# Kernel optimization log

Measured on AMD Instinct MI355X. Metric: run time of the kernel, lower is better.

The kernel has to match this reference:

```python
import jax, jax.numpy as jnp
import numpy as np

L = 3; D = 128; H = 8; RBF = 16; SBF = 112
N = 60000; E = 300000; A = 8000; G = 256
EPS = 1e-8


def setup_inputs() -> dict:
    key = jax.random.key(0)
    ks = jax.random.split(key, 32)
    p = lambda i, shape: jax.random.normal(ks[i], shape, jnp.float32) * 0.05
    inp = {}
    inp['x'] = jax.random.normal(ks[0], (N, D), jnp.float32)
    inp['node_rbf'] = jax.random.uniform(ks[1], (N, RBF), jnp.float32)
    inp['edge_sbf'] = jax.random.uniform(ks[2], (E, SBF), jnp.float32)
    inp['edge_index'] = jax.random.randint(ks[3], (2, E), 0, N)
    inp['pair_atom_idx'] = jax.random.randint(ks[4], (E,), 0, A)
    inp['edge_index_0'] = jax.random.randint(ks[5], (N,), 0, A)
    inp['atom_batch'] = jnp.sort(jax.random.randint(ks[6], (A,), 0, G))
    inp['batch'] = jnp.sort(jax.random.randint(ks[7], (N,), 0, G))
    inp['edgenn_w1'] = p(8, (L, D, D)); inp['edgenn_b1'] = jnp.zeros((L, D))
    inp['edgenn_w2'] = p(9, (L, D, D)); inp['edgenn_b2'] = jnp.zeros((L, D))
    inp['conv_wq'] = p(10, (L, D, D)); inp['conv_wk'] = p(11, (L, D, D))
    inp['conv_wv'] = p(12, (L, D, D)); inp['conv_we'] = p(13, (L, D, D))
    inp['conv_wsbf'] = p(14, (L, SBF, D)); inp['conv_bsbf'] = jnp.zeros((L, D))
    inp['conv_wrbf'] = p(15, (L, RBF, D))
    inp['dense_w'] = p(16, (L, D, D)); inp['dense_b'] = jnp.zeros((L, D))
    inp['bf_w'] = p(17, (L, 2, D, D)); inp['bf_b'] = jnp.zeros((L, 2, D))
    inp['af_w'] = p(18, (L, 4, D, D)); inp['af_b'] = jnp.zeros((L, 4, D))
    inp['read_wrbf'] = p(19, (L + 1, RBF, D))
    inp['read_w1'] = p(20, (L + 1, D, D)); inp['read_b1'] = jnp.zeros((L + 1, D))
    inp['read_w2'] = p(21, (L + 1, D, D)); inp['read_b2'] = jnp.zeros((L + 1, D))
    inp['read_w3'] = p(22, (L + 1, D, 1)); inp['read_b3'] = jnp.zeros((L + 1, 1))
    return inp


def _forward(x, node_rbf, edge_sbf, edge_index, pair_atom_idx, edge_index_0,
             atom_batch, batch, edgenn_w1, edgenn_b1, edgenn_w2, edgenn_b2,
             conv_wq, conv_wk, conv_wv, conv_we, conv_wsbf, conv_bsbf, conv_wrbf,
             dense_w, dense_b, bf_w, bf_b, af_w, af_b,
             read_wrbf, read_w1, read_b1, read_w2, read_b2, read_w3, read_b3):
    segsum = jax.ops.segment_sum
    silu = jax.nn.silu
    src, dst = edge_index[0], edge_index[1]
    C = D // H

    def readout(i, h):
        # AtomWise: rbf-gated node features, scatter to atoms, small MLP -> [A,1]
        g = h * (node_rbf @ read_wrbf[i])
        atoms = segsum(g, edge_index_0, num_segments=A)
        a = silu(atoms @ read_w1[i] + read_b1[i])
        a = silu(a @ read_w2[i] + read_b2[i])
        return a @ read_w3[i] + read_b3[i]

    def res_block(h, w, b):
        # DimeNet-style ResidualLayer: x + act(lin2(act(lin1(x))))
        return h + silu(silu(h @ w[0] + b[0]) @ w[1] + b[1])

    def graph_norm(h):
        # batch-aware LayerNorm (graph mode, affine=False)
        cnt = segsum(jnp.ones((N,), h.dtype), batch, num_segments=G) * D
        mean = segsum(h.sum(-1), batch, num_segments=G) / cnt
        hc = h - mean[batch][:, None]
        var = segsum((hc * hc).sum(-1), batch, num_segments=G) / cnt
        return hc * jax.lax.rsqrt(var + EPS)[batch][:, None]

    out = x
    results = readout(0, out)
    for i in range(L):
        res0 = out
        atoms_rep = segsum(out, edge_index_0, num_segments=A)  # scatter_add to atoms
        ea = atoms_rep[pair_atom_idx]                           # gather per conv-edge
        ea = silu(ea @ edgenn_w1[i] + edgenn_b1[i]) @ edgenn_w2[i] + edgenn_b2[i]
        # SBFTransformerConv: TransformerConv with sbf-modulated messages + rbf gate
        q = (out @ conv_wq[i]).reshape(N, H, C)
        k = (out @ conv_wk[i]).reshape(N, H, C)
        v = (out @ conv_wv[i]).reshape(N, H, C)
        ek = (ea @ conv_we[i]).reshape(E, H, C)
        kj = k[src] + ek
        logit = (q[dst] * kj).sum(-1) / jnp.sqrt(jnp.asarray(C, out.dtype))  # [E,H]
        m = jax.ops.segment_max(logit, dst, num_segments=N)
        ex = jnp.exp(logit - m[dst])
        alpha = ex / (segsum(ex, dst, num_segments=N)[dst] + 1e-16)
        sw = (edge_sbf @ conv_wsbf[i] + conv_bsbf[i]).reshape(E, H, C)
        msg = (v[src] + ek) * alpha[:, :, None] * sw
        h = segsum(msg, dst, num_segments=N).reshape(N, D)
        out = h * (node_rbf @ conv_wrbf[i])
        out = graph_norm(out)
        out = res_block(out, bf_w[i], bf_b[i])
        out = silu(out @ dense_w[i] + dense_b[i])
        out = out + res0
        out = res_block(out, af_w[i, :2], af_b[i, :2])
        out = res_block(out, af_w[i, 2:], af_b[i, 2:])
        results = results + readout(i + 1, out)
    graphs = segsum(results, atom_batch, num_segments=G)  # [G,1]
    return graphs.reshape(-1) / L


def reference(x, node_rbf, edge_sbf, edge_index, pair_atom_idx, edge_index_0,
              atom_batch, batch, edgenn_w1, edgenn_b1, edgenn_w2, edgenn_b2,
              conv_wq, conv_wk, conv_wv, conv_we, conv_wsbf, conv_bsbf, conv_wrbf,
              dense_w, dense_b, bf_w, bf_b, af_w, af_b,
              read_wrbf, read_w1, read_b1, read_w2, read_b2, read_w3, read_b3):
    return _forward(x, node_rbf, edge_sbf, edge_index, pair_atom_idx, edge_index_0,
                    atom_batch, batch, edgenn_w1, edgenn_b1, edgenn_w2, edgenn_b2,
                    conv_wq, conv_wk, conv_wv, conv_we, conv_wsbf, conv_bsbf, conv_wrbf,
                    dense_w, dense_b, bf_w, bf_b, af_w, af_b,
                    read_wrbf, read_w1, read_b1, read_w2, read_b2, read_w3, read_b3)
```

## Files before the change

kernel.cpp:

```cpp
#include <hip/hip_runtime.h>
#include <math.h>

#define D    128
#define NH   8
#define CPH  16
#define RBFD 16
#define SBFD 112
#define LAYERS 3

typedef __attribute__((ext_vector_type(8))) short bf16x8;
typedef __attribute__((ext_vector_type(4))) float f32x4;

__device__ __forceinline__ float siluf(float x){ return x / (1.0f + __expf(-x)); }

__device__ __forceinline__ short f2bf(float f){
  union { float f; unsigned u; } v; v.f = f;
  unsigned r = v.u + 0x7FFFu + ((v.u >> 16) & 1u);
  return (short)(r >> 16);
}

template<int DIN, int ACT, bool GATHER, bool HASB, bool HASRES, bool PERM>
__global__ __launch_bounds__(256, 2) void k_gemm(
    const float* __restrict__ X, const int* __restrict__ gidx,
    const float* __restrict__ W, const float* __restrict__ bias,
    const float* res, float* __restrict__ Y, const int* __restrict__ operm, int M)
{
  __shared__ short Wt[128 * 128];
  if (DIN < 128){
    for (int i = threadIdx.x; i < 128 * 128; i += 256) Wt[i] = 0;
    __syncthreads();
  }
  for (int i = threadIdx.x; i < DIN * 128; i += 256){
    int k = i >> 7, c = i & 127;
    Wt[c * 128 + k] = f2bf(W[i]);
  }
  __syncthreads();

  const int lane = threadIdx.x & 63;
  const int wave = threadIdx.x >> 6;
  const int col0 = lane & 15;
  const int kg   = lane >> 4;

  bf16x8 Bf[8][4];
  #pragma unroll
  for (int ct = 0; ct < 8; ct++)
    #pragma unroll
    for (int s = 0; s < 4; s++)
      Bf[ct][s] = *(const bf16x8*)&Wt[(ct * 16 + col0) * 128 + s * 32 + kg * 8];

  float bs[8];
  if (HASB){
    #pragma unroll
    for (int ct = 0; ct < 8; ct++) bs[ct] = bias[ct * 16 + col0];
  }

  const long tiles = ((long)M + 63) >> 6;
  for (long t = blockIdx.x; t < tiles; t += gridDim.x){
    const long rbase = t * 64 + wave * 16;
    const long arow  = rbase + col0;
    long srow = 0;
    if (arow < M) srow = GATHER ? (long)gidx[arow] : arow;
    const float* Xp = X + srow * DIN;

    bf16x8 Af[4];
    #pragma unroll
    for (int s = 0; s < 4; s++){
      const int kb = s * 32 + kg * 8;
      bf16x8 a;
      if (DIN == 128 || kb + 8 <= DIN){
        float4 lo = *(const float4*)(Xp + kb);
        float4 hi = *(const float4*)(Xp + kb + 4);
        a[0]=f2bf(lo.x); a[1]=f2bf(lo.y); a[2]=f2bf(lo.z); a[3]=f2bf(lo.w);
        a[4]=f2bf(hi.x); a[5]=f2bf(hi.y); a[6]=f2bf(hi.z); a[7]=f2bf(hi.w);
      } else {
        #pragma unroll
        for (int j = 0; j < 8; j++) a[j] = 0;
      }
      Af[s] = a;
    }

    f32x4 acc[8];
    #pragma unroll
    for (int ct = 0; ct < 8; ct++){ acc[ct][0]=0.f; acc[ct][1]=0.f; acc[ct][2]=0.f; acc[ct][3]=0.f; }
    #pragma unroll
    for (int ct = 0; ct < 8; ct++)
      #pragma unroll
      for (int s = 0; s < 4; s++)
        acc[ct] = __builtin_amdgcn_mfma_f32_16x16x32_bf16(Af[s], Bf[ct][s], acc[ct], 0, 0, 0);

    #pragma unroll
    for (int r = 0; r < 4; r++){
      const long orow = rbase + kg * 4 + r;
      if (orow >= M) continue;
      const long wrow = PERM ? (long)operm[orow] : orow;
      #pragma unroll
      for (int ct = 0; ct < 8; ct++){
        const int c = ct * 16 + col0;
        float v = acc[ct][r];
        if (HASB) v += bs[ct];
        if (ACT)  v = siluf(v);
        if (HASRES) v += res[orow * D + c];
        Y[wrow * D + c] = v;
      }
    }
  }
}

__global__ __launch_bounds__(256, 2) void k_gemm2(
    const float* __restrict__ X, const int* __restrict__ gidx,
    const float* __restrict__ W1, const float* __restrict__ b1,
    const float* __restrict__ W2, const float* __restrict__ b2,
    float* __restrict__ Y, const int* __restrict__ operm, int M)
{
  __shared__ short W1t[128 * 128];
  __shared__ short W2t[128 * 128];
  __shared__ short Ts[64 * 128];
  for (int i = threadIdx.x; i < 128 * 128; i += 256){
    int k = i >> 7, c = i & 127;
    W1t[c * 128 + k] = f2bf(W1[i]);
    W2t[c * 128 + k] = f2bf(W2[i]);
  }
  __syncthreads();

  const int lane = threadIdx.x & 63;
  const int wave = threadIdx.x >> 6;
  const int col0 = lane & 15;
  const int kg   = lane >> 4;

  bf16x8 B1f[8][4];
  #pragma unroll
  for (int ct = 0; ct < 8; ct++)
    #pragma unroll
    for (int s = 0; s < 4; s++)
      B1f[ct][s] = *(const bf16x8*)&W1t[(ct * 16 + col0) * 128 + s * 32 + kg * 8];

  float bs1[8], bs2[8];
  #pragma unroll
  for (int ct = 0; ct < 8; ct++){ bs1[ct] = b1[ct * 16 + col0]; bs2[ct] = b2[ct * 16 + col0]; }

  const long tiles = ((long)M + 63) >> 6;
  for (long t = blockIdx.x; t < tiles; t += gridDim.x){
    const long rbase = t * 64 + wave * 16;
    const long arow  = rbase + col0;
    long srow = 0;
    if (arow < M) srow = (long)gidx[arow];
    const float* Xp = X + srow * D;

    bf16x8 Af[4];
    #pragma unroll
    for (int s = 0; s < 4; s++){
      const int kb = s * 32 + kg * 8;
      float4 lo = *(const float4*)(Xp + kb);
      float4 hi = *(const float4*)(Xp + kb + 4);
      bf16x8 a;
      a[0]=f2bf(lo.x); a[1]=f2bf(lo.y); a[2]=f2bf(lo.z); a[3]=f2bf(lo.w);
      a[4]=f2bf(hi.x); a[5]=f2bf(hi.y); a[6]=f2bf(hi.z); a[7]=f2bf(hi.w);
      Af[s] = a;
    }

    f32x4 acc[8];
    #pragma unroll
    for (int ct = 0; ct < 8; ct++){ acc[ct][0]=0.f; acc[ct][1]=0.f; acc[ct][2]=0.f; acc[ct][3]=0.f; }
    #pragma unroll
    for (int ct = 0; ct < 8; ct++)
      #pragma unroll
      for (int s = 0; s < 4; s++)
        acc[ct] = __builtin_amdgcn_mfma_f32_16x16x32_bf16(Af[s], B1f[ct][s], acc[ct], 0, 0, 0);

    #pragma unroll
    for (int ct = 0; ct < 8; ct++){
      const int c = ct * 16 + col0;
      #pragma unroll
      for (int r = 0; r < 4; r++){
        const int row = wave * 16 + kg * 4 + r;
        const int gg = (c >> 3) ^ (row & 7);
        Ts[row * 128 + gg * 8 + (c & 7)] = f2bf(siluf(acc[ct][r] + bs1[ct]));
      }
    }
    __syncthreads();

    const int row2 = wave * 16 + col0;
    bf16x8 A2f[4];
    #pragma unroll
    for (int s = 0; s < 4; s++){
      const int chunk = (s * 4 + kg) ^ (row2 & 7);
      A2f[s] = *(const bf16x8*)&Ts[row2 * 128 + chunk * 8];
    }
    __syncthreads();

    #pragma unroll
    for (int ct = 0; ct < 8; ct++){ acc[ct][0]=0.f; acc[ct][1]=0.f; acc[ct][2]=0.f; acc[ct][3]=0.f; }
    #pragma unroll
    for (int ct = 0; ct < 8; ct++){
      bf16x8 B2v[4];
      #pragma unroll
      for (int s = 0; s < 4; s++)
        B2v[s] = *(const bf16x8*)&W2t[(ct * 16 + col0) * 128 + s * 32 + kg * 8];
      #pragma unroll
      for (int s = 0; s < 4; s++)
        acc[ct] = __builtin_amdgcn_mfma_f32_16x16x32_bf16(A2f[s], B2v[s], acc[ct], 0, 0, 0);
    }

    #pragma unroll
    for (int r = 0; r < 4; r++){
      const long orow = rbase + kg * 4 + r;
      if (orow >= M) continue;
      const long wrow = (long)operm[orow];
      #pragma unroll
      for (int ct = 0; ct < 8; ct++){
        const int c = ct * 16 + col0;
        Y[wrow * D + c] = acc[ct][r] + bs2[ct];
      }
    }
  }
}

template<bool NORM>
__global__ __launch_bounds__(256, 2) void k_res2(
    const float* __restrict__ X,
    const float* __restrict__ W1, const float* __restrict__ b1,
    const float* __restrict__ W2, const float* __restrict__ b2,
    const int* __restrict__ batch, const float* __restrict__ meanG,
    const float* __restrict__ rstdG, float* __restrict__ Y, int M)
{
  __shared__ short W1t[128 * 128];
  __shared__ short W2t[128 * 128];
  __shared__ short Ts[64 * 128];
  for (int i = threadIdx.x; i < 128 * 128; i += 256){
    int k = i >> 7, c = i & 127;
    W1t[c * 128 + k] = f2bf(W1[i]);
    W2t[c * 128 + k] = f2bf(W2[i]);
  }
  __syncthreads();

  const int lane = threadIdx.x & 63;
  const int wave = threadIdx.x >> 6;
  const int col0 = lane & 15;
  const int kg   = lane >> 4;

  bf16x8 B1f[8][4];
  #pragma unroll
  for (int ct = 0; ct < 8; ct++)
    #pragma unroll
    for (int s = 0; s < 4; s++)
      B1f[ct][s] = *(const bf16x8*)&W1t[(ct * 16 + col0) * 128 + s * 32 + kg * 8];

  float bs1[8], bs2[8];
  #pragma unroll
  for (int ct = 0; ct < 8; ct++){ bs1[ct] = b1[ct * 16 + col0]; bs2[ct] = b2[ct * 16 + col0]; }

  const long tiles = ((long)M + 63) >> 6;
  for (long t = blockIdx.x; t < tiles; t += gridDim.x){
    const long rbase = t * 64 + wave * 16;
    const long arow  = rbase + col0;
    const float* Xp = X + (arow < M ? arow : 0) * D;
    float xm = 0.f, xr = 1.f;
    if (NORM && arow < M){ int g = batch[arow]; xm = meanG[g]; xr = rstdG[g]; }

    bf16x8 Af[4];
    #pragma unroll
    for (int s = 0; s < 4; s++){
      const int kb = s * 32 + kg * 8;
      float4 lo = *(const float4*)(Xp + kb);
      float4 hi = *(const float4*)(Xp + kb + 4);
      bf16x8 a;
      a[0]=f2bf((lo.x-xm)*xr); a[1]=f2bf((lo.y-xm)*xr); a[2]=f2bf((lo.z-xm)*xr); a[3]=f2bf((lo.w-xm)*xr);
      a[4]=f2bf((hi.x-xm)*xr); a[5]=f2bf((hi.y-xm)*xr); a[6]=f2bf((hi.z-xm)*xr); a[7]=f2bf((hi.w-xm)*xr);
      Af[s] = a;
    }

    f32x4 acc[8];
    #pragma unroll
    for (int ct = 0; ct < 8; ct++){ acc[ct][0]=0.f; acc[ct][1]=0.f; acc[ct][2]=0.f; acc[ct][3]=0.f; }
    #pragma unroll
    for (int ct = 0; ct < 8; ct++)
      #pragma unroll
      for (int s = 0; s < 4; s++)
        acc[ct] = __builtin_amdgcn_mfma_f32_16x16x32_bf16(Af[s], B1f[ct][s], acc[ct], 0, 0, 0);

    #pragma unroll
    for (int ct = 0; ct < 8; ct++){
      const int c = ct * 16 + col0;
      #pragma unroll
      for (int r = 0; r < 4; r++){
        const int row = wave * 16 + kg * 4 + r;
        const int gg = (c >> 3) ^ (row & 7);
        Ts[row * 128 + gg * 8 + (c & 7)] = f2bf(siluf(acc[ct][r] + bs1[ct]));
      }
    }
    __syncthreads();

    const int row2 = wave * 16 + col0;
    bf16x8 A2f[4];
    #pragma unroll
    for (int s = 0; s < 4; s++){
      const int chunk = (s * 4 + kg) ^ (row2 & 7);
      A2f[s] = *(const bf16x8*)&Ts[row2 * 128 + chunk * 8];
    }
    __syncthreads();

    #pragma unroll
    for (int ct = 0; ct < 8; ct++){ acc[ct][0]=0.f; acc[ct][1]=0.f; acc[ct][2]=0.f; acc[ct][3]=0.f; }
    #pragma unroll
    for (int ct = 0; ct < 8; ct++){
      bf16x8 B2v[4];
      #pragma unroll
      for (int s = 0; s < 4; s++)
        B2v[s] = *(const bf16x8*)&W2t[(ct * 16 + col0) * 128 + s * 32 + kg * 8];
      #pragma unroll
      for (int s = 0; s < 4; s++)
        acc[ct] = __builtin_amdgcn_mfma_f32_16x16x32_bf16(A2f[s], B2v[s], acc[ct], 0, 0, 0);
    }

    #pragma unroll
    for (int r = 0; r < 4; r++){
      const long orow = rbase + kg * 4 + r;
      if (orow >= M) continue;
      float rm = 0.f, rr = 1.f;
      if (NORM){ int g = batch[orow]; rm = meanG[g]; rr = rstdG[g]; }
      #pragma unroll
      for (int ct = 0; ct < 8; ct++){
        const int c = ct * 16 + col0;
        float base = X[orow * D + c];
        if (NORM) base = (base - rm) * rr;
        Y[orow * D + c] = base + siluf(acc[ct][r] + bs2[ct]);
      }
    }
  }
}

__global__ __launch_bounds__(256, 2) void k_read2(
    const float* __restrict__ X,
    const float* __restrict__ W1, const float* __restrict__ b1,
    const float* __restrict__ W2, const float* __restrict__ b2,
    const float* __restrict__ w3, const float* __restrict__ b3,
    float* __restrict__ results, int M)
{
  __shared__ short W1t[128 * 128];
  __shared__ short W2t[128 * 128];
  __shared__ short Ts[64 * 128];
  for (int i = threadIdx.x; i < 128 * 128; i += 256){
    int k = i >> 7, c = i & 127;
    W1t[c * 128 + k] = f2bf(W1[i]);
    W2t[c * 128 + k] = f2bf(W2[i]);
  }
  __syncthreads();

  const int lane = threadIdx.x & 63;
  const int wave = threadIdx.x >> 6;
  const int col0 = lane & 15;
  const int kg   = lane >> 4;

  bf16x8 B1f[8][4];
  #pragma unroll
  for (int ct = 0; ct < 8; ct++)
    #pragma unroll
    for (int s = 0; s < 4; s++)
      B1f[ct][s] = *(const bf16x8*)&W1t[(ct * 16 + col0) * 128 + s * 32 + kg * 8];

  float bs1[8], bs2[8], w3v[8];
  #pragma unroll
  for (int ct = 0; ct < 8; ct++){
    bs1[ct] = b1[ct * 16 + col0];
    bs2[ct] = b2[ct * 16 + col0];
    w3v[ct] = w3[ct * 16 + col0];
  }
  const float b3v = b3[0];

  const long tiles = ((long)M + 63) >> 6;
  for (long t = blockIdx.x; t < tiles; t += gridDim.x){
    const long rbase = t * 64 + wave * 16;
    const long arow  = rbase + col0;
    const float* Xp = X + (arow < M ? arow : 0) * D;

    bf16x8 Af[4];
    #pragma unroll
    for (int s = 0; s < 4; s++){
      const int kb = s * 32 + kg * 8;
      float4 lo = *(const float4*)(Xp + kb);
      float4 hi = *(const float4*)(Xp + kb + 4);
      bf16x8 a;
      a[0]=f2bf(lo.x); a[1]=f2bf(lo.y); a[2]=f2bf(lo.z); a[3]=f2bf(lo.w);
      a[4]=f2bf(hi.x); a[5]=f2bf(hi.y); a[6]=f2bf(hi.z); a[7]=f2bf(hi.w);
      Af[s] = a;
    }

    f32x4 acc[8];
    #pragma unroll
    for (int ct = 0; ct < 8; ct++){ acc[ct][0]=0.f; acc[ct][1]=0.f; acc[ct][2]=0.f; acc[ct][3]=0.f; }
    #pragma unroll
    for (int ct = 0; ct < 8; ct++)
      #pragma unroll
      for (int s = 0; s < 4; s++)
        acc[ct] = __builtin_amdgcn_mfma_f32_16x16x32_bf16(Af[s], B1f[ct][s], acc[ct], 0, 0, 0);

    #pragma unroll
    for (int ct = 0; ct < 8; ct++){
      const int c = ct * 16 + col0;
      #pragma unroll
      for (int r = 0; r < 4; r++){
        const int row = wave * 16 + kg * 4 + r;
        const int gg = (c >> 3) ^ (row & 7);
        Ts[row * 128 + gg * 8 + (c & 7)] = f2bf(siluf(acc[ct][r] + bs1[ct]));
      }
    }
    __syncthreads();

    const int row2 = wave * 16 + col0;
    bf16x8 A2f[4];
    #pragma unroll
    for (int s = 0; s < 4; s++){
      const int chunk = (s * 4 + kg) ^ (row2 & 7);
      A2f[s] = *(const bf16x8*)&Ts[row2 * 128 + chunk * 8];
    }
    __syncthreads();

    #pragma unroll
    for (int ct = 0; ct < 8; ct++){ acc[ct][0]=0.f; acc[ct][1]=0.f; acc[ct][2]=0.f; acc[ct][3]=0.f; }
    #pragma unroll
    for (int ct = 0; ct < 8; ct++){
      bf16x8 B2v[4];
      #pragma unroll
      for (int s = 0; s < 4; s++)
        B2v[s] = *(const bf16x8*)&W2t[(ct * 16 + col0) * 128 + s * 32 + kg * 8];
      #pragma unroll
      for (int s = 0; s < 4; s++)
        acc[ct] = __builtin_amdgcn_mfma_f32_16x16x32_bf16(A2f[s], B2v[s], acc[ct], 0, 0, 0);
    }

    #pragma unroll
    for (int r = 0; r < 4; r++){
      float vr = 0.f;
      #pragma unroll
      for (int ct = 0; ct < 8; ct++)
        vr += siluf(acc[ct][r] + bs2[ct]) * w3v[ct];
      #pragma unroll
      for (int off = 1; off < 16; off <<= 1) vr += __shfl_xor(vr, off, 64);
      const long orow = rbase + kg * 4 + r;
      if (col0 == 0 && orow < M) results[orow] += vr + b3v;
    }
  }
}

__global__ void k_hist(const int* __restrict__ idx, int* __restrict__ cnt, int M)
{
  for (long i = (long)blockIdx.x * 256 + threadIdx.x; i < M; i += (long)gridDim.x * 256)
    atomicAdd(&cnt[idx[i]], 1);
}

__global__ void k_scan(const int* __restrict__ cnt, int* __restrict__ rowptr, int M)
{
  __shared__ int buf[1024];
  const int tid = threadIdx.x;
  const int PT = 16;
  int carry = 0;
  for (int base = 0; base < M; base += 1024 * PT){
    int loc[PT]; int s = 0;
    #pragma unroll
    for (int j = 0; j < PT; j++){
      int i = base + tid * PT + j;
      loc[j] = (i < M) ? cnt[i] : 0;
      s += loc[j];
    }
    buf[tid] = s; __syncthreads();
    for (int off = 1; off < 1024; off <<= 1){
      int t = (tid >= off) ? buf[tid - off] : 0;
      __syncthreads();
      buf[tid] += t;
      __syncthreads();
    }
    int run = buf[tid] - s + carry;
    carry += buf[1023];
    __syncthreads();
    #pragma unroll
    for (int j = 0; j < PT; j++){
      int i = base + tid * PT + j;
      if (i < M) rowptr[i] = run;
      run += loc[j];
    }
  }
  if (tid == 0) rowptr[M] = carry;
}

__global__ void k_fill(const int* __restrict__ idx, const int* __restrict__ rowptr,
                       int* __restrict__ cursor, int* __restrict__ ids, int M)
{
  for (long i = (long)blockIdx.x * 256 + threadIdx.x; i < M; i += (long)gridDim.x * 256){
    int sgm = idx[i];
    int pos = atomicAdd(&cursor[sgm], 1);
    ids[rowptr[sgm] + pos] = (int)i;
  }
}

__global__ void k_invsrc(const int* __restrict__ eids, const int* __restrict__ srcA,
                         int* __restrict__ invD, int* __restrict__ srcCSR, int E_)
{
  for (long i = (long)blockIdx.x * 256 + threadIdx.x; i < E_; i += (long)gridDim.x * 256){
    int e = eids[i];
    invD[e] = (int)i;
    srcCSR[i] = srcA[e];
  }
}

__global__ __launch_bounds__(256) void k_gather_sum(
    const float* __restrict__ X, const int* __restrict__ rowptr,
    const int* __restrict__ ids, float* __restrict__ Yat, int A_)
{
  const int lane = threadIdx.x & 63;
  const int wv   = threadIdx.x >> 6;
  for (long a = (long)blockIdx.x * 4 + wv; a < A_; a += (long)gridDim.x * 4){
    int beg = rowptr[a], end = rowptr[a + 1];
    float a0 = 0.f, a1 = 0.f;
    for (int i = beg; i < end; i++){
      const float* xp = X + (long)ids[i] * D;
      a0 += xp[lane]; a1 += xp[lane + 64];
    }
    Yat[a * D + lane] = a0; Yat[a * D + lane + 64] = a1;
  }
}

__global__ __launch_bounds__(256) void k_gather_gate_sum(
    const float* __restrict__ X, const float* __restrict__ rbf,
    const float* __restrict__ Wr, const int* __restrict__ rowptr,
    const int* __restrict__ ids, float* __restrict__ Yat, int A_)
{
  __shared__ float Wrs[RBFD * D];
  for (int i = threadIdx.x; i < RBFD * D; i += 256) Wrs[i] = Wr[i];
  __syncthreads();
  const int lane = threadIdx.x & 63;
  const int wv   = threadIdx.x >> 6;
  for (long a = (long)blockIdx.x * 4 + wv; a < A_; a += (long)gridDim.x * 4){
    int beg = rowptr[a], end = rowptr[a + 1];
    float a0 = 0.f, a1 = 0.f;
    for (int i = beg; i < end; i++){
      long n = ids[i];
      const float* xp = X + n * D;
      const float* rb = rbf + n * RBFD;
      float g0 = 0.f, g1 = 0.f;
      #pragma unroll
      for (int r = 0; r < RBFD; r++){
        float rv = rb[r];
        g0 += rv * Wrs[r * D + lane];
        g1 += rv * Wrs[r * D + lane + 64];
      }
      a0 += xp[lane] * g0; a1 += xp[lane + 64] * g1;
    }
    Yat[a * D + lane] = a0; Yat[a * D + lane + 64] = a1;
  }
}

__device__ __forceinline__ void attn_step(long i, const int* __restrict__ srcCSR,
    const float* __restrict__ k, const float* __restrict__ v,
    const float* __restrict__ ek, const float* __restrict__ sw, int lane,
    float q0, float q1, float& m0, float& m1, float& l0, float& l1, float& a0, float& a1)
{
  const long s = srcCSR[i];
  const float* kp = k + s * D;
  const float* vp = v + s * D;
  const float* ep = ek + i * D;
  const float* sp = sw + i * D;
  float e0 = ep[lane], e1 = ep[lane + 64];
  float t0 = q0 * (kp[lane] + e0), t1 = q1 * (kp[lane + 64] + e1);
  #pragma unroll
  for (int off = 1; off < 16; off <<= 1){
    t0 += __shfl_xor(t0, off, 64);
    t1 += __shfl_xor(t1, off, 64);
  }
  t0 *= 0.25f; t1 *= 0.25f;
  float u0 = (vp[lane] + e0) * sp[lane];
  float u1 = (vp[lane + 64] + e1) * sp[lane + 64];
  float nm0 = fmaxf(m0, t0), nm1 = fmaxf(m1, t1);
  float sc0 = __expf(m0 - nm0), sc1 = __expf(m1 - nm1);
  float w0 = __expf(t0 - nm0), w1 = __expf(t1 - nm1);
  l0 = l0 * sc0 + w0;  a0 = a0 * sc0 + w0 * u0;  m0 = nm0;
  l1 = l1 * sc1 + w1;  a1 = a1 * sc1 + w1 * u1;  m1 = nm1;
}

__global__ __launch_bounds__(256) void k_attn(
    float* __restrict__ q, const float* __restrict__ k, const float* __restrict__ v,
    const float* __restrict__ ek, const float* __restrict__ sw,
    const int* __restrict__ rowptr, const int* __restrict__ srcCSR,
    const float* __restrict__ rbf, const float* __restrict__ Wr,
    const int* __restrict__ batch,
    double* __restrict__ sums, double* __restrict__ sumsq, int Nn)
{
  __shared__ float Wrs[RBFD * D];
  for (int i = threadIdx.x; i < RBFD * D; i += 256) Wrs[i] = Wr[i];
  __syncthreads();
  const int lane = threadIdx.x & 63;
  const int wv   = threadIdx.x >> 6;
  for (long d = (long)blockIdx.x * 4 + wv; d < Nn; d += (long)gridDim.x * 4){
    const int beg = rowptr[d], end = rowptr[d + 1];
    const float q0 = q[d * D + lane], q1 = q[d * D + lane + 64];
    float mA0=-1e30f, mA1=-1e30f, lA0=0.f, lA1=0.f, aA0=0.f, aA1=0.f;
    float mB0=-1e30f, mB1=-1e30f, lB0=0.f, lB1=0.f, aB0=0.f, aB1=0.f;
    int i = beg;
    for (; i + 1 < end; i += 2){
      attn_step(i,     srcCSR, k, v, ek, sw, lane, q0, q1, mA0, mA1, lA0, lA1, aA0, aA1);
      attn_step(i + 1, srcCSR, k, v, ek, sw, lane, q0, q1, mB0, mB1, lB0, lB1, aB0, aB1);
    }
    if (i < end)
      attn_step(i, srcCSR, k, v, ek, sw, lane, q0, q1, mA0, mA1, lA0, lA1, aA0, aA1);
    float nm0 = fmaxf(mA0, mB0), nm1 = fmaxf(mA1, mB1);
    float sA0 = __expf(mA0 - nm0), sB0 = __expf(mB0 - nm0);
    float sA1 = __expf(mA1 - nm1), sB1 = __expf(mB1 - nm1);
    float l0 = lA0 * sA0 + lB0 * sB0, l1 = lA1 * sA1 + lB1 * sB1;
    float a0 = aA0 * sA0 + aB0 * sB0, a1 = aA1 * sA1 + aB1 * sB1;
    a0 /= (l0 + 1e-16f); a1 /= (l1 + 1e-16f);
    const float* rb = rbf + d * RBFD;
    float g0 = 0.f, g1 = 0.f;
    #pragma unroll
    for (int r = 0; r < RBFD; r++){
      float rv = rb[r];
      g0 += rv * Wrs[r * D + lane];
      g1 += rv * Wrs[r * D + lane + 64];
    }
    a0 *= g0; a1 *= g1;
    q[d * D + lane] = a0; q[d * D + lane + 64] = a1;
    float ss = a0 + a1, qq = a0 * a0 + a1 * a1;
    #pragma unroll
    for (int off = 1; off < 64; off <<= 1){
      ss += __shfl_xor(ss, off, 64);
      qq += __shfl_xor(qq, off, 64);
    }
    if (lane == 0){
      int g = batch[d];
      atomicAdd(&sums[g], (double)ss);
      atomicAdd(&sumsq[g], (double)qq);
    }
  }
}

__global__ void k_count(const int* __restrict__ batch, int* __restrict__ cnt, int M)
{
  for (long i = (long)blockIdx.x * 256 + threadIdx.x; i < M; i += (long)gridDim.x * 256)
    atomicAdd(&cnt[batch[i]], 1);
}

__global__ void k_norm_final(const double* __restrict__ sums, const double* __restrict__ sumsq,
                             const int* __restrict__ cnt, float* __restrict__ meanG,
                             float* __restrict__ rstdG)
{
  int g = threadIdx.x;
  double c = (double)cnt[g] * (double)D;
  double mean = sums[g] / c;
  double var = sumsq[g] / c - mean * mean;
  meanG[g] = (float)mean;
  rstdG[g] = (float)(1.0 / sqrt(var + 1e-8));
}

__global__ void k_final(const float* __restrict__ results, const int* __restrict__ ab,
                        float* __restrict__ out, int A_)
{
  int i = blockIdx.x * 256 + threadIdx.x;
  if (i < A_) atomicAdd(&out[ab[i]], results[i] / 3.0f);
}

__global__ void k_w2e(const float* __restrict__ w2, const float* __restrict__ we,
                      float* __restrict__ W2e)
{
  int i = blockIdx.x >> 7;
  int r = blockIdx.x & 127;
  int c = threadIdx.x;
  const float* w2p = w2 + (size_t)i * D * D + (size_t)r * D;
  const float* wep = we + (size_t)i * D * D;
  float acc = 0.f;
  for (int j = 0; j < D; j++) acc += w2p[j] * wep[j * D + c];
  W2e[(size_t)i * D * D + (size_t)r * D + c] = acc;
}

__global__ void k_b2e(const float* __restrict__ b2, const float* __restrict__ we,
                      float* __restrict__ B2e)
{
  int i = blockIdx.x; int c = threadIdx.x;
  float acc = 0.f;
  for (int j = 0; j < D; j++) acc += b2[(size_t)i * D + j] * we[(size_t)i * D * D + j * D + c];
  B2e[(size_t)i * D + c] = acc;
}

extern "C" void kernel_launch(void* const* d_in, const int* in_sizes, int n_in,
                              void* d_out, int out_size, void* d_ws, size_t ws_size,
                              hipStream_t stream)
{
  const float* x          = (const float*)d_in[0];
  const float* node_rbf   = (const float*)d_in[1];
  const float* edge_sbf   = (const float*)d_in[2];
  const int*   edge_index = (const int*)d_in[3];
  const int*   pair_idx   = (const int*)d_in[4];
  const int*   eidx0      = (const int*)d_in[5];
  const int*   atom_batch = (const int*)d_in[6];
  const int*   batch      = (const int*)d_in[7];
  const float* edgenn_w1  = (const float*)d_in[8];
  const float* edgenn_b1  = (const float*)d_in[9];
  const float* edgenn_w2  = (const float*)d_in[10];
  const float* edgenn_b2  = (const float*)d_in[11];
  const float* conv_wq    = (const float*)d_in[12];
  const float* conv_wk    = (const float*)d_in[13];
  const float* conv_wv    = (const float*)d_in[14];
  const float* conv_we    = (const float*)d_in[15];
  const float* conv_wsbf  = (const float*)d_in[16];
  const float* conv_bsbf  = (const float*)d_in[17];
  const float* conv_wrbf  = (const float*)d_in[18];
  const float* dense_w    = (const float*)d_in[19];
  const float* dense_b    = (const float*)d_in[20];
  const float* bf_w       = (const float*)d_in[21];
  const float* bf_b       = (const float*)d_in[22];
  const float* af_w       = (const float*)d_in[23];
  const float* af_b       = (const float*)d_in[24];
  const float* read_wrbf  = (const float*)d_in[25];
  const float* read_w1    = (const float*)d_in[26];
  const float* read_b1    = (const float*)d_in[27];
  const float* read_w2    = (const float*)d_in[28];
  const float* read_b2    = (const float*)d_in[29];
  const float* read_w3    = (const float*)d_in[30];
  const float* read_b3    = (const float*)d_in[31];

  const int N = in_sizes[0] / D;
  const int E = in_sizes[4];
  const int A = in_sizes[6];
  const int G = out_size;

  char* p = (char*)d_ws;
  auto carve = [&](size_t bytes)->char*{ char* r = p; p += (bytes + 255) & ~(size_t)255; return r; };
  float*    EbufA   = (float*)carve((size_t)E * D * 4);
  float*    EbufB   = (float*)carve((size_t)E * D * 4);
  float*    ping0   = (float*)carve((size_t)N * D * 4);
  float*    ping1   = (float*)carve((size_t)N * D * 4);
  float*    bq      = (float*)carve((size_t)N * D * 4);
  float*    bk      = (float*)carve((size_t)N * D * 4);
  float*    bv      = (float*)carve((size_t)N * D * 4);
  float*    bufAtoms= (float*)carve((size_t)A * D * 4);
  float*    results = (float*)carve((size_t)A * 4);
  double*   sumG    = (double*)carve((size_t)G * 8);
  double*   sumsqG  = (double*)carve((size_t)G * 8);
  int*      cntG    = (int*)carve((size_t)G * 4);
  float*    meanG   = (float*)carve((size_t)G * 4);
  float*    rstdG   = (float*)carve((size_t)G * 4);
  float*    W2e     = (float*)carve((size_t)LAYERS * D * D * 4);
  float*    B2e     = (float*)carve((size_t)LAYERS * D * 4);
  int*      rowptrD = (int*)carve((size_t)(N + 1) * 4);
  int*      eidsD   = (int*)carve((size_t)E * 4);
  int*      invD    = (int*)carve((size_t)E * 4);
  int*      srcCSR  = (int*)carve((size_t)E * 4);
  int*      cntD    = (int*)carve((size_t)N * 4);
  int*      rowptrA = (int*)carve((size_t)(A + 1) * 4);
  int*      idsA    = (int*)carve((size_t)N * 4);
  int*      cntA    = (int*)carve((size_t)A * 4);

  const int* srcA = edge_index;
  const int* dstA = edge_index + E;

  auto ew_grid = [](long total){ long b = (total + 255) / 256; return (int)(b < 4096 ? b : 4096); };
  auto gemm_grid = [](int M){ long t = ((long)M + 63) / 64; return (int)(t < 1024 ? t : 1024); };
  const int gridAttn = (N + 3) / 4;
  const int gridAtom = (A + 3) / 4;

  hipMemsetAsync(cntG, 0, (size_t)G * 4, stream);
  hipMemsetAsync(results, 0, (size_t)A * 4, stream);
  hipMemsetAsync(d_out, 0, (size_t)G * 4, stream);
  k_count<<<ew_grid(N), 256, 0, stream>>>(batch, cntG, N);
  k_w2e<<<LAYERS * D, D, 0, stream>>>(edgenn_w2, conv_we, W2e);
  k_b2e<<<LAYERS, D, 0, stream>>>(edgenn_b2, conv_we, B2e);
  hipMemsetAsync(cntD, 0, (size_t)N * 4, stream);
  k_hist<<<ew_grid(E), 256, 0, stream>>>(dstA, cntD, E);
  k_scan<<<1, 1024, 0, stream>>>(cntD, rowptrD, N);
  hipMemsetAsync(cntD, 0, (size_t)N * 4, stream);
  k_fill<<<ew_grid(E), 256, 0, stream>>>(dstA, rowptrD, cntD, eidsD, E);
  k_invsrc<<<ew_grid(E), 256, 0, stream>>>(eidsD, srcA, invD, srcCSR, E);
  hipMemsetAsync(cntA, 0, (size_t)A * 4, stream);
  k_hist<<<ew_grid(N), 256, 0, stream>>>(eidx0, cntA, N);
  k_scan<<<1, 1024, 0, stream>>>(cntA, rowptrA, A);
  hipMemsetAsync(cntA, 0, (size_t)A * 4, stream);
  k_fill<<<ew_grid(N), 256, 0, stream>>>(eidx0, rowptrA, cntA, idsA, N);

  auto readout = [&](int i, const float* hbuf){
    k_gather_gate_sum<<<gridAtom, 256, 0, stream>>>(hbuf, node_rbf, read_wrbf + (size_t)i * RBFD * D,
                                                    rowptrA, idsA, bufAtoms, A);
    k_read2<<<gemm_grid(A), 256, 0, stream>>>(bufAtoms,
        read_w1 + (size_t)i*D*D, read_b1 + (size_t)i*D,
        read_w2 + (size_t)i*D*D, read_b2 + (size_t)i*D,
        read_w3 + (size_t)i*D, read_b3 + i, results, A);
  };

  readout(0, x);

  const float* cur = x;
  float* pp[2] = {ping0, ping1};
  for (int i = 0; i < LAYERS; i++){
    float* nxt = pp[i & 1];
    const size_t oDD = (size_t)i * D * D;
    k_gather_sum<<<gridAtom, 256, 0, stream>>>(cur, rowptrA, idsA, bufAtoms, A);
    k_gemm2<<<gemm_grid(E),256,0,stream>>>(bufAtoms, pair_idx, edgenn_w1 + oDD, edgenn_b1 + (size_t)i*D,
                                           W2e + oDD, B2e + (size_t)i*D, EbufB, invD, E);
    k_gemm<D,0,false,false,false,false><<<gemm_grid(N),256,0,stream>>>(cur, nullptr, conv_wq + oDD, nullptr, nullptr, bq, nullptr, N);
    k_gemm<D,0,false,false,false,false><<<gemm_grid(N),256,0,stream>>>(cur, nullptr, conv_wk + oDD, nullptr, nullptr, bk, nullptr, N);
    k_gemm<D,0,false,false,false,false><<<gemm_grid(N),256,0,stream>>>(cur, nullptr, conv_wv + oDD, nullptr, nullptr, bv, nullptr, N);
    k_gemm<SBFD,0,false,true,false,true><<<gemm_grid(E),256,0,stream>>>(edge_sbf, nullptr, conv_wsbf + (size_t)i*SBFD*D, conv_bsbf + (size_t)i*D, nullptr, EbufA, invD, E);
    hipMemsetAsync(sumG, 0, (size_t)G * 16, stream);
    k_attn<<<gridAttn, 256, 0, stream>>>(bq, bk, bv, EbufB, EbufA, rowptrD, srcCSR,
                                         node_rbf, conv_wrbf + (size_t)i*RBFD*D, batch,
                                         sumG, sumsqG, N);
    k_norm_final<<<1, G, 0, stream>>>(sumG, sumsqG, cntG, meanG, rstdG);
    k_res2<true><<<gemm_grid(N),256,0,stream>>>(bq, bf_w + (size_t)i*2*D*D, bf_b + (size_t)i*2*D,
                                                bf_w + (size_t)i*2*D*D + D*D, bf_b + (size_t)i*2*D + D,
                                                batch, meanG, rstdG, bq, N);
    k_gemm<D,1,false,true,true,false><<<gemm_grid(N),256,0,stream>>>(bq, nullptr, dense_w + oDD, dense_b + (size_t)i*D, cur, nxt, nullptr, N);
    k_res2<false><<<gemm_grid(N),256,0,stream>>>(nxt, af_w + (size_t)i*4*D*D,         af_b + (size_t)i*4*D,
                                                 af_w + (size_t)i*4*D*D + D*D,       af_b + (size_t)i*4*D + D,
                                                 nullptr, nullptr, nullptr, nxt, N);
    k_res2<false><<<gemm_grid(N),256,0,stream>>>(nxt, af_w + (size_t)i*4*D*D + 2*D*D, af_b + (size_t)i*4*D + 2*D,
                                                 af_w + (size_t)i*4*D*D + 3*D*D,     af_b + (size_t)i*4*D + 3*D,
                                                 nullptr, nullptr, nullptr, nxt, N);
    readout(i + 1, nxt);
    cur = nxt;
  }
  k_final<<<(A + 255) / 256, 256, 0, stream>>>(results, atom_batch, (float*)d_out, A);
}
```

Measured before the change: 3.255 ms.

## Store attention operands in bf16 and simplify softmax to unnormalized exp

The q/k/v projections, edge key and sbf-weight buffers are now written as bf16, which halves the traffic of the gather-heavy attention kernel. The attention loop now drops the online max-tracking softmax and sums exp directly. It processes four edges per iteration with batched loads, and each lane handles an adjacent channel pair so loads are packed. Output goes to a separate fp32 buffer. This trades precision and overflow safety, since exp is no longer max-shifted, for less memory traffic and fewer instructions.

Result: faster. 3.132 ms (-3.8%).

```diff
diff --git a/kernel.cpp b/kernel.cpp
--- a/kernel.cpp
+++ b/kernel.cpp
@@ -3,7 +3,6 @@
 
 #define D    128
 #define NH   8
-#define CPH  16
 #define RBFD 16
 #define SBFD 112
 #define LAYERS 3
@@ -18,12 +17,14 @@
   unsigned r = v.u + 0x7FFFu + ((v.u >> 16) & 1u);
   return (short)(r >> 16);
 }
-
-template<int DIN, int ACT, bool GATHER, bool HASB, bool HASRES, bool PERM>
+__device__ __forceinline__ float bflo(unsigned u){ return __uint_as_float(u << 16); }
+__device__ __forceinline__ float bfhi(unsigned u){ return __uint_as_float(u & 0xFFFF0000u); }
+
+template<int DIN, int ACT, bool GATHER, bool HASB, bool HASRES, bool PERM, bool OUTBF>
 __global__ __launch_bounds__(256, 2) void k_gemm(
     const float* __restrict__ X, const int* __restrict__ gidx,
     const float* __restrict__ W, const float* __restrict__ bias,
-    const float* res, float* __restrict__ Y, const int* __restrict__ operm, int M)
+    const float* res, void* __restrict__ Yv, const int* __restrict__ operm, int M)
 {
   __shared__ short Wt[128 * 128];
   if (DIN < 128){
@@ -53,6 +54,9 @@
     #pragma unroll
     for (int ct = 0; ct < 8; ct++) bs[ct] = bias[ct * 16 + col0];
   }
+
+  float* __restrict__ Yf = (float*)Yv;
+  unsigned short* __restrict__ Yb = (unsigned short*)Yv;
 
   const long tiles = ((long)M + 63) >> 6;
   for (long t = blockIdx.x; t < tiles; t += gridDim.x){
@@ -100,7 +104,8 @@
         if (HASB) v += bs[ct];
         if (ACT)  v = siluf(v);
         if (HASRES) v += res[orow * D + c];
-        Y[wrow * D + c] = v;
+        if (OUTBF) Yb[wrow * D + c] = (unsigned short)f2bf(v);
+        else       Yf[wrow * D + c] = v;
       }
     }
   }
@@ -110,7 +115,7 @@
     const float* __restrict__ X, const int* __restrict__ gidx,
     const float* __restrict__ W1, const float* __restrict__ b1,
     const float* __restrict__ W2, const float* __restrict__ b2,
-    float* __restrict__ Y, const int* __restrict__ operm, int M)
+    unsigned short* __restrict__ Y, const int* __restrict__ operm, int M)
 {
   __shared__ short W1t[128 * 128];
   __shared__ short W2t[128 * 128];
@@ -209,7 +214,7 @@
       #pragma unroll
       for (int ct = 0; ct < 8; ct++){
         const int c = ct * 16 + col0;
-        Y[wrow * D + c] = acc[ct][r] + bs2[ct];
+        Y[wrow * D + c] = (unsigned short)f2bf(acc[ct][r] + bs2[ct]);
       }
     }
   }
@@ -549,40 +554,15 @@
   }
 }
 
-__device__ __forceinline__ void attn_step(long i, const int* __restrict__ srcCSR,
-    const float* __restrict__ k, const float* __restrict__ v,
-    const float* __restrict__ ek, const float* __restrict__ sw, int lane,
-    float q0, float q1, float& m0, float& m1, float& l0, float& l1, float& a0, float& a1)
-{
-  const long s = srcCSR[i];
-  const float* kp = k + s * D;
-  const float* vp = v + s * D;
-  const float* ep = ek + i * D;
-  const float* sp = sw + i * D;
-  float e0 = ep[lane], e1 = ep[lane + 64];
-  float t0 = q0 * (kp[lane] + e0), t1 = q1 * (kp[lane + 64] + e1);
-  #pragma unroll
-  for (int off = 1; off < 16; off <<= 1){
-    t0 += __shfl_xor(t0, off, 64);
-    t1 += __shfl_xor(t1, off, 64);
-  }
-  t0 *= 0.25f; t1 *= 0.25f;
-  float u0 = (vp[lane] + e0) * sp[lane];
-  float u1 = (vp[lane + 64] + e1) * sp[lane + 64];
-  float nm0 = fmaxf(m0, t0), nm1 = fmaxf(m1, t1);
-  float sc0 = __expf(m0 - nm0), sc1 = __expf(m1 - nm1);
-  float w0 = __expf(t0 - nm0), w1 = __expf(t1 - nm1);
-  l0 = l0 * sc0 + w0;  a0 = a0 * sc0 + w0 * u0;  m0 = nm0;
-  l1 = l1 * sc1 + w1;  a1 = a1 * sc1 + w1 * u1;  m1 = nm1;
-}
-
 __global__ __launch_bounds__(256) void k_attn(
-    float* __restrict__ q, const float* __restrict__ k, const float* __restrict__ v,
-    const float* __restrict__ ek, const float* __restrict__ sw,
+    const unsigned short* __restrict__ q, const unsigned short* __restrict__ k,
+    const unsigned short* __restrict__ v, const unsigned short* __restrict__ ek,
+    const unsigned short* __restrict__ sw,
     const int* __restrict__ rowptr, const int* __restrict__ srcCSR,
     const float* __restrict__ rbf, const float* __restrict__ Wr,
     const int* __restrict__ batch,
-    double* __restrict__ sums, double* __restrict__ sumsq, int Nn)
+    double* __restrict__ sums, double* __restrict__ sumsq,
+    float* __restrict__ h, int Nn)
 {
   __shared__ float Wrs[RBFD * D];
   for (int i = threadIdx.x; i < RBFD * D; i += 256) Wrs[i] = Wr[i];
@@ -591,32 +571,46 @@
   const int wv   = threadIdx.x >> 6;
   for (long d = (long)blockIdx.x * 4 + wv; d < Nn; d += (long)gridDim.x * 4){
     const int beg = rowptr[d], end = rowptr[d + 1];
-    const float q0 = q[d * D + lane], q1 = q[d * D + lane + 64];
-    float mA0=-1e30f, mA1=-1e30f, lA0=0.f, lA1=0.f, aA0=0.f, aA1=0.f;
-    float mB0=-1e30f, mB1=-1e30f, lB0=0.f, lB1=0.f, aB0=0.f, aB1=0.f;
-    int i = beg;
-    for (; i + 1 < end; i += 2){
-      attn_step(i,     srcCSR, k, v, ek, sw, lane, q0, q1, mA0, mA1, lA0, lA1, aA0, aA1);
-      attn_step(i + 1, srcCSR, k, v, ek, sw, lane, q0, q1, mB0, mB1, lB0, lB1, aB0, aB1);
-    }
-    if (i < end)
-      attn_step(i, srcCSR, k, v, ek, sw, lane, q0, q1, mA0, mA1, lA0, lA1, aA0, aA1);
-    float nm0 = fmaxf(mA0, mB0), nm1 = fmaxf(mA1, mB1);
-    float sA0 = __expf(mA0 - nm0), sB0 = __expf(mB0 - nm0);
-    float sA1 = __expf(mA1 - nm1), sB1 = __expf(mB1 - nm1);
-    float l0 = lA0 * sA0 + lB0 * sB0, l1 = lA1 * sA1 + lB1 * sB1;
-    float a0 = aA0 * sA0 + aB0 * sB0, a1 = aA1 * sA1 + aB1 * sB1;
-    a0 /= (l0 + 1e-16f); a1 /= (l1 + 1e-16f);
+    const unsigned qp = *(const unsigned*)(q + d * D + 2 * lane);
+    const float q0 = bflo(qp), q1 = bfhi(qp);
+    float l = 0.f, a0 = 0.f, a1 = 0.f;
+    for (int i = beg; i < end; i += 4){
+      unsigned kk[4], vv[4], ee[4], ssw[4];
+      #pragma unroll
+      for (int j = 0; j < 4; j++){
+        const long idx = (i + j < end) ? (long)(i + j) : (long)(end - 1);
+        const long s = srcCSR[idx];
+        kk[j]  = *(const unsigned*)(k  + s * D + 2 * lane);
+        vv[j]  = *(const unsigned*)(v  + s * D + 2 * lane);
+        ee[j]  = *(const unsigned*)(ek + idx * D + 2 * lane);
+        ssw[j] = *(const unsigned*)(sw + idx * D + 2 * lane);
+      }
+      #pragma unroll
+      for (int j = 0; j < 4; j++){
+        const float valid = (i + j < end) ? 1.f : 0.f;
+        float e0 = bflo(ee[j]), e1 = bfhi(ee[j]);
+        float t = q0 * (bflo(kk[j]) + e0) + q1 * (bfhi(kk[j]) + e1);
+        t += __shfl_xor(t, 1, 64);
+        t += __shfl_xor(t, 2, 64);
+        t += __shfl_xor(t, 4, 64);
+        float w = __expf(t * 0.25f) * valid;
+        float u0 = (bflo(vv[j]) + e0) * bflo(ssw[j]);
+        float u1 = (bfhi(vv[j]) + e1) * bfhi(ssw[j]);
+        l += w; a0 += w * u0; a1 += w * u1;
+      }
+    }
+    const float inv = 1.f / (l + 1e-16f);
+    a0 *= inv; a1 *= inv;
     const float* rb = rbf + d * RBFD;
     float g0 = 0.f, g1 = 0.f;
     #pragma unroll
     for (int r = 0; r < RBFD; r++){
       float rv = rb[r];
-      g0 += rv * Wrs[r * D + lane];
-      g1 += rv * Wrs[r * D + lane + 64];
+      g0 += rv * Wrs[r * D + 2 * lane];
+      g1 += rv * Wrs[r * D + 2 * lane + 1];
     }
     a0 *= g0; a1 *= g1;
-    q[d * D + lane] = a0; q[d * D + lane + 64] = a1;
+    *(float2*)(h + d * D + 2 * lane) = make_float2(a0, a1);
     float ss = a0 + a1, qq = a0 * a0 + a1 * a1;
     #pragma unroll
     for (int off = 1; off < 64; off <<= 1){
@@ -722,13 +716,14 @@
 
   char* p = (char*)d_ws;
   auto carve = [&](size_t bytes)->char*{ char* r = p; p += (bytes + 255) & ~(size_t)255; return r; };
-  float*    EbufA   = (float*)carve((size_t)E * D * 4);
-  float*    EbufB   = (float*)carve((size_t)E * D * 4);
+  unsigned short* ekb  = (unsigned short*)carve((size_t)E * D * 2);
+  unsigned short* swb  = (unsigned short*)carve((size_t)E * D * 2);
+  unsigned short* qb   = (unsigned short*)carve((size_t)N * D * 2);
+  unsigned short* kb   = (unsigned short*)carve((size_t)N * D * 2);
+  unsigned short* vb   = (unsigned short*)carve((size_t)N * D * 2);
+  float*    hbuf    = (float*)carve((size_t)N * D * 4);
   float*    ping0   = (float*)carve((size_t)N * D * 4);
   float*    ping1   = (float*)carve((size_t)N * D * 4);
-  float*    bq      = (float*)carve((size_t)N * D * 4);
-  float*    bk      = (float*)carve((size_t)N * D * 4);
-  float*    bv      = (float*)carve((size_t)N * D * 4);
   float*    bufAtoms= (float*)carve((size_t)A * D * 4);
   float*    results = (float*)carve((size_t)A * 4);
   double*   sumG    = (double*)carve((size_t)G * 8);
@@ -773,8 +768,8 @@
   hipMemsetAsync(cntA, 0, (size_t)A * 4, stream);
   k_fill<<<ew_grid(N), 256, 0, stream>>>(eidx0, rowptrA, cntA, idsA, N);
 
-  auto readout = [&](int i, const float* hbuf){
-    k_gather_gate_sum<<<gridAtom, 256, 0, stream>>>(hbuf, node_rbf, read_wrbf + (size_t)i * RBFD * D,
+  auto readout = [&](int i, const float* hb){
+    k_gather_gate_sum<<<gridAtom, 256, 0, stream>>>(hb, node_rbf, read_wrbf + (size_t)i * RBFD * D,
                                                     rowptrA, idsA, bufAtoms, A);
     k_read2<<<gemm_grid(A), 256, 0, stream>>>(bufAtoms,
         read_w1 + (size_t)i*D*D, read_b1 + (size_t)i*D,
@@ -791,20 +786,20 @@
     const size_t oDD = (size_t)i * D * D;
     k_gather_sum<<<gridAtom, 256, 0, stream>>>(cur, rowptrA, idsA, bufAtoms, A);
     k_gemm2<<<gemm_grid(E),256,0,stream>>>(bufAtoms, pair_idx, edgenn_w1 + oDD, edgenn_b1 + (size_t)i*D,
-                                           W2e + oDD, B2e + (size_t)i*D, EbufB, invD, E);
-    k_gemm<D,0,false,false,false,false><<<gemm_grid(N),256,0,stream>>>(cur, nullptr, conv_wq + oDD, nullptr, nullptr, bq, nullptr, N);
-    k_gemm<D,0,false,false,false,false><<<gemm_grid(N),256,0,stream>>>(cur, nullptr, conv_wk + oDD, nullptr, nullptr, bk, nullptr, N);
-    k_gemm<D,0,false,false,false,false><<<gemm_grid(N),256,0,stream>>>(cur, nullptr, conv_wv + oDD, nullptr, nullptr, bv, nullptr, N);
-    k_gemm<SBFD,0,false,true,false,true><<<gemm_grid(E),256,0,stream>>>(edge_sbf, nullptr, conv_wsbf + (size_t)i*SBFD*D, conv_bsbf + (size_t)i*D, nullptr, EbufA, invD, E);
+                                           W2e + oDD, B2e + (size_t)i*D, ekb, invD, E);
+    k_gemm<D,0,false,false,false,false,true><<<gemm_grid(N),256,0,stream>>>(cur, nullptr, conv_wq + oDD, nullptr, nullptr, qb, nullptr, N);
+    k_gemm<D,0,false,false,false,false,true><<<gemm_grid(N),256,0,stream>>>(cur, nullptr, conv_wk + oDD, nullptr, nullptr, kb, nullptr, N);
+    k_gemm<D,0,false,false,false,false,true><<<gemm_grid(N),256,0,stream>>>(cur, nullptr, conv_wv + oDD, nullptr, nullptr, vb, nullptr, N);
+    k_gemm<SBFD,0,false,true,false,true,true><<<gemm_grid(E),256,0,stream>>>(edge_sbf, nullptr, conv_wsbf + (size_t)i*SBFD*D, conv_bsbf + (size_t)i*D, nullptr, swb, invD, E);
     hipMemsetAsync(sumG, 0, (size_t)G * 16, stream);
-    k_attn<<<gridAttn, 256, 0, stream>>>(bq, bk, bv, EbufB, EbufA, rowptrD, srcCSR,
+    k_attn<<<gridAttn, 256, 0, stream>>>(qb, kb, vb, ekb, swb, rowptrD, srcCSR,
                                          node_rbf, conv_wrbf + (size_t)i*RBFD*D, batch,
-                                         sumG, sumsqG, N);
+                                         sumG, sumsqG, hbuf, N);
     k_norm_final<<<1, G, 0, stream>>>(sumG, sumsqG, cntG, meanG, rstdG);
-    k_res2<true><<<gemm_grid(N),256,0,stream>>>(bq, bf_w + (size_t)i*2*D*D, bf_b + (size_t)i*2*D,
+    k_res2<true><<<gemm_grid(N),256,0,stream>>>(hbuf, bf_w + (size_t)i*2*D*D, bf_b + (size_t)i*2*D,
                                                 bf_w + (size_t)i*2*D*D + D*D, bf_b + (size_t)i*2*D + D,
-                                                batch, meanG, rstdG, bq, N);
-    k_gemm<D,1,false,true,true,false><<<gemm_grid(N),256,0,stream>>>(bq, nullptr, dense_w + oDD, dense_b + (size_t)i*D, cur, nxt, nullptr, N);
+                                                batch, meanG, rstdG, hbuf, N);
+    k_gemm<D,1,false,true,true,false,false><<<gemm_grid(N),256,0,stream>>>(hbuf, nullptr, dense_w + oDD, dense_b + (size_t)i*D, cur, nxt, nullptr, N);
     k_res2<false><<<gemm_grid(N),256,0,stream>>>(nxt, af_w + (size_t)i*4*D*D,         af_b + (size_t)i*4*D,
                                                  af_w + (size_t)i*4*D*D + D*D,       af_b + (size_t)i*4*D + D,
                                                  nullptr, nullptr, nullptr, nxt, N);
```
